# Kernel tuning notes

Hardware: AMD Instinct MI355X
Metric: run time of the kernel (lower is better)

Reference implementation:

```python
import jax, jax.numpy as jnp
import numpy as np

D_MODEL = 512; NHEAD = 8; D_FF = 2048
B = 8; C = 64; P = 128
HALF = D_MODEL // 2        # per-branch embed dim (256)
H_HALF = NHEAD // 2        # per-branch heads (4)
HD = HALF // H_HALF        # per-branch head dim (64)
ROPE_BASE = 10000.0
THETA_SCALE = 2.0 * np.pi
LN_EPS = 1e-5; RMS_EPS = 1e-8


def setup_inputs():
    ks = jax.random.split(jax.random.key(0), 16)
    w = lambda k, s: jax.random.normal(k, s, jnp.float32) * 0.02
    return {
        "src": jax.random.normal(ks[0], (B, C, P, D_MODEL), jnp.float32),
        "coords": jax.random.normal(ks[1], (C, 3), jnp.float32),
        "q_attn": w(ks[2], (D_MODEL,)), "rms_attn": jnp.ones((D_MODEL,), jnp.float32),
        "proj_attn_w": w(ks[3], (D_MODEL, D_MODEL)), "proj_attn_b": jnp.zeros((D_MODEL,), jnp.float32),
        "q_ffn": w(ks[4], (D_MODEL,)), "rms_ffn": jnp.ones((D_MODEL,), jnp.float32),
        "proj_ffn_w": w(ks[5], (D_MODEL, D_MODEL)), "proj_ffn_b": jnp.zeros((D_MODEL,), jnp.float32),
        "ln1_w": jnp.ones((D_MODEL,), jnp.float32), "ln1_b": jnp.zeros((D_MODEL,), jnp.float32),
        "ln2_w": jnp.ones((D_MODEL,), jnp.float32), "ln2_b": jnp.zeros((D_MODEL,), jnp.float32),
        "qkv_s_w": w(ks[6], (3 * HALF, HALF)), "qkv_s_b": jnp.zeros((3 * HALF,), jnp.float32),
        "out_s_w": w(ks[7], (HALF, HALF)), "out_s_b": jnp.zeros((HALF,), jnp.float32),
        "qkv_t_w": w(ks[8], (3 * HALF, HALF)), "qkv_t_b": jnp.zeros((3 * HALF,), jnp.float32),
        "out_t_w": w(ks[9], (HALF, HALF)), "out_t_b": jnp.zeros((HALF,), jnp.float32),
        "w1": w(ks[10], (D_FF, D_MODEL)), "b1": jnp.zeros((D_FF,), jnp.float32),
        "w2": w(ks[11], (D_MODEL, D_FF)), "b2": jnp.zeros((D_MODEL,), jnp.float32),
    }


def _rmsnorm(x, w):
    return x / jnp.sqrt(jnp.mean(x * x, axis=-1, keepdims=True) + RMS_EPS) * w


def _layernorm(x, w, b):
    m = jnp.mean(x, axis=-1, keepdims=True)
    v = jnp.mean((x - m) ** 2, axis=-1, keepdims=True)
    return (x - m) / jnp.sqrt(v + LN_EPS) * w + b


def _attn_residual(src, q, norm_w, proj_w, proj_b):
    # sources = [src] stacked on a leading n-axis (n=1) as in AttentionResidual
    V = src[None]                                  # (n, B, C, P, D)
    K = _rmsnorm(V, norm_w)
    logits = jnp.einsum('d,nbcpd->nbcp', q, K)
    wgt = jax.nn.softmax(logits, axis=0)
    out = jnp.einsum('nbcp,nbcpd->bcpd', wgt, V)
    return out @ proj_w.T + proj_b


def _build_freqs(half, dtype):
    idx = jnp.arange(half, dtype=dtype)
    return 1.0 / ROPE_BASE ** (idx / max(half, 1))


def _coord_rope(coords, half):
    # coords: (L, 3); returns cos, sin of shape (1, 1, L, half)
    axis_ids = jnp.arange(half) % 3
    c = coords - jnp.mean(coords, axis=0, keepdims=True)
    r = jnp.linalg.norm(c, axis=-1)
    c = c / jnp.maximum(jnp.max(r), 1e-6)
    freqs = _build_freqs(half, coords.dtype)
    theta = THETA_SCALE * (c[:, axis_ids] * freqs[None, :])   # (L, half)
    return jnp.cos(theta)[None, None], jnp.sin(theta)[None, None]


def _index_rope(L, half, dtype):
    freqs = _build_freqs(half, dtype)
    pos = jnp.arange(L, dtype=dtype)[:, None]
    theta = pos * freqs[None, :]                               # (L, half)
    return jnp.cos(theta)[None, None], jnp.sin(theta)[None, None]


def _apply_rope(q, k, cos, sin):
    half = q.shape[-1] // 2
    q1, q2 = q[..., :half], q[..., half:]
    k1, k2 = k[..., :half], k[..., half:]
    qr = jnp.concatenate([q1 * cos - q2 * sin, q1 * sin + q2 * cos], axis=-1)
    kr = jnp.concatenate([k1 * cos - k2 * sin, k1 * sin + k2 * cos], axis=-1)
    return qr, kr


def _mha(x, w_qkv, b_qkv, w_o, b_o, H, cos, sin):
    Bx, L, E = x.shape
    Hd = E // H
    qkv = x @ w_qkv.T + b_qkv
    q, k, v = jnp.split(qkv, 3, axis=-1)
    q = q.reshape(Bx, L, H, Hd).transpose(0, 2, 1, 3)   # (B, H, L, Hd)
    k = k.reshape(Bx, L, H, Hd).transpose(0, 2, 1, 3)
    v = v.reshape(Bx, L, H, Hd).transpose(0, 2, 1, 3)
    q, k = _apply_rope(q, k, cos, sin)
    scores = jnp.einsum('bhld,bhmd->bhlm', q, k) * (Hd ** -0.5)
    attn = jax.nn.softmax(scores, axis=-1)
    out = jnp.einsum('bhlm,bhmd->bhld', attn, v)
    out = out.transpose(0, 2, 1, 3).reshape(Bx, L, E)
    return out @ w_o.T + b_o


def reference(src, coords, q_attn, rms_attn, proj_attn_w, proj_attn_b,
              q_ffn, rms_ffn, proj_ffn_w, proj_ffn_b,
              ln1_w, ln1_b, ln2_w, ln2_b,
              qkv_s_w, qkv_s_b, out_s_w, out_s_b,
              qkv_t_w, qkv_t_b, out_t_w, out_t_b,
              w1, b1, w2, b2):
    Bx, Cx, Px, D = src.shape
    half = D // 2
    # --- attention block (pre-norm, attention-residual shortcut) ---
    res1 = _attn_residual(src, q_attn, rms_attn, proj_attn_w, proj_attn_b)
    x = _layernorm(src, ln1_w, ln1_b)
    # spatial branch: attention over channels with coordinate RoPE
    xs = x[..., :half].transpose(0, 2, 1, 3).reshape(Bx * Px, Cx, half)
    cos_s, sin_s = _coord_rope(coords, HD // 2)
    ys = _mha(xs, qkv_s_w, qkv_s_b, out_s_w, out_s_b, H_HALF, cos_s, sin_s)
    ys = ys.reshape(Bx, Px, Cx, half).transpose(0, 2, 1, 3)
    # temporal branch: attention over patches with index RoPE
    xt = x[..., half:].reshape(Bx * Cx, Px, half)
    cos_t, sin_t = _index_rope(Px, HD // 2, src.dtype)
    yt = _mha(xt, qkv_t_w, qkv_t_b, out_t_w, out_t_b, H_HALF, cos_t, sin_t)
    yt = yt.reshape(Bx, Cx, Px, half)
    x = res1 + jnp.concatenate([ys, yt], axis=-1)
    # --- FFN block ---
    res2 = _attn_residual(x, q_ffn, rms_ffn, proj_ffn_w, proj_ffn_b)
    y = _layernorm(x, ln2_w, ln2_b)
    ff = jax.nn.gelu(y @ w1.T + b1, approximate=False) @ w2.T + b2
    return res2 + ff
```

## Files before the change

### kernel.cpp

```cpp
#include <hip/hip_runtime.h>
#include <math.h>
#include <type_traits>

using u16 = unsigned short;
using u32 = unsigned int;

typedef __bf16 bf16x8 __attribute__((ext_vector_type(8)));
typedef float f32x4 __attribute__((ext_vector_type(4)));

__device__ __forceinline__ float lof(u32 u) { u32 x = u << 16; float f; __builtin_memcpy(&f, &x, 4); return f; }
__device__ __forceinline__ float hif(u32 u) { u32 x = u & 0xffff0000u; float f; __builtin_memcpy(&f, &x, 4); return f; }
__device__ __forceinline__ u16 f2bf(float f) {
  u32 u; __builtin_memcpy(&u, &f, 4);
  u32 r = u + 0x7fffu + ((u >> 16) & 1u);
  return (u16)(r >> 16);
}
__device__ __forceinline__ u32 pack2(float a, float b) { return (u32)f2bf(a) | ((u32)f2bf(b) << 16); }
__device__ __forceinline__ float bf2f(u16 s) { u32 x = ((u32)s) << 16; float f; __builtin_memcpy(&f, &x, 4); return f; }
__device__ __forceinline__ float elem(const u32* arr, int j) { u32 u = arr[j >> 1]; return (j & 1) ? hif(u) : lof(u); }

__device__ __forceinline__ void gload_lds16(const u16* g, u16* l) {
  __builtin_amdgcn_global_load_lds((const __attribute__((address_space(1))) void*)g,
                                   (__attribute__((address_space(3))) void*)l, 16, 0, 0);
}

__device__ __forceinline__ float gelu_f(float x) {
  float x3 = x * x * x;
  float u = fmaf(x3, 0.07135481283f, 1.5957691216f * x);
  float e = __expf(u);
  float r = __builtin_amdgcn_rcpf(e + 1.0f);
  return x * e * r;
}

#define NTOK 65536

#define WB_PA   0
#define WB_PF   262144
#define WB_QS   524288
#define WB_QT   720896
#define WB_OS   917504
#define WB_OT   983040
#define WB_W1   1048576
#define WB_W2F  2097152
#define WB_TOT  3407872

#define UC_US 0
#define UC_CS 768
#define UC_UT 1536
#define UC_CT 2304
#define UC_U1 3072
#define UC_C1 5120
#define UC_BC 7168

constexpr size_t O_WB  = 0;
constexpr size_t O_TAB = 6815744;
constexpr size_t O_ST1 = 6864896;
constexpr size_t O_ST2 = 7389184;
constexpr size_t O_UC  = 7913472;
constexpr size_t O_X   = 7944192;
constexpr size_t O_HB  = O_X + (size_t)NTOK * 512 * 2;

__global__ __launch_bounds__(256) void convert_weights_kernel(
    const float* __restrict__ pa, const float* __restrict__ pf,
    const float* __restrict__ qs, const float* __restrict__ qt,
    const float* __restrict__ os_, const float* __restrict__ ot,
    const float* __restrict__ w1, const float* __restrict__ w2,
    const float* __restrict__ ln1w, const float* __restrict__ ln2w,
    u16* __restrict__ dst)
{
  int i = blockIdx.x * 256 + threadIdx.x;
  if (i >= WB_TOT) return;
  float v;
  if (i < 262144)       { v = pa[i]; }
  else if (i < 524288)  { v = pf[i - 262144]; }
  else if (i < 720896)  { int l = i - 524288;  v = qs[l] * ln1w[l & 255]; }
  else if (i < 917504)  { int l = i - 720896;  v = qt[l] * ln1w[256 + (l & 255)]; }
  else if (i < 983040)  { v = os_[i - 917504]; }
  else if (i < 1048576) { v = ot[i - 983040]; }
  else if (i < 2097152) { int l = i - 1048576; v = w1[l] * ln2w[l & 511]; }
  else {
    int l = i - 2097152; int row = l / 2560, col = l - row * 2560;
    v = (col < 2048) ? w2[row * 2048 + col] : pf[row * 512 + (col - 2048)];
  }
  dst[i] = f2bf(v);
}

__global__ __launch_bounds__(256) void ucvec_kernel(
    const float* __restrict__ qs, const float* __restrict__ qt, const float* __restrict__ w1,
    const float* __restrict__ ln1w, const float* __restrict__ ln1b,
    const float* __restrict__ ln2w, const float* __restrict__ ln2b,
    const float* __restrict__ b2, const float* __restrict__ pfb,
    float* __restrict__ uc)
{
  int j = blockIdx.x * 256 + threadIdx.x;
  if (j < 768) {
    float u = 0.f, c = 0.f;
    for (int k = 0; k < 256; k++) { float w = qs[j * 256 + k]; u += ln1w[k] * w; c += ln1b[k] * w; }
    uc[UC_US + j] = u; uc[UC_CS + j] = c;
  } else if (j < 1536) {
    int jj = j - 768; float u = 0.f, c = 0.f;
    for (int k = 0; k < 256; k++) { float w = qt[jj * 256 + k]; u += ln1w[256 + k] * w; c += ln1b[256 + k] * w; }
    uc[UC_UT + jj] = u; uc[UC_CT + jj] = c;
  } else if (j < 3584) {
    int jj = j - 1536; float u = 0.f, c = 0.f;
    for (int k = 0; k < 512; k++) { float w = w1[jj * 512 + k]; u += ln2w[k] * w; c += ln2b[k] * w; }
    uc[UC_U1 + jj] = u; uc[UC_C1 + jj] = c;
  } else if (j < 4096) {
    int jj = j - 3584;
    uc[UC_BC + jj] = b2[jj] + pfb[jj];
  }
}

__global__ __launch_bounds__(256) void rope_tables_kernel(const float* __restrict__ coords, float* __restrict__ tab)
{
  __shared__ float cs[192];
  __shared__ float mean3[3];
  __shared__ float rmax;
  int t = threadIdx.x;
  if (t < 192) cs[t] = coords[t];
  __syncthreads();
  if (t < 3) { float s = 0.f; for (int i = 0; i < 64; i++) s += cs[i * 3 + t]; mean3[t] = s * (1.0f / 64.0f); }
  __syncthreads();
  if (t < 192) cs[t] -= mean3[t % 3];
  __syncthreads();
  if (t == 0) {
    float mx = 0.f;
    for (int i = 0; i < 64; i++) {
      float x = cs[i * 3], y = cs[i * 3 + 1], z = cs[i * 3 + 2];
      mx = fmaxf(mx, sqrtf(x * x + y * y + z * z));
    }
    rmax = fmaxf(mx, 1e-6f);
  }
  __syncthreads();
  float inv = 1.0f / rmax;
  for (int e = t; e < 2048; e += 256) {
    int c = e >> 5, j = e & 31;
    float freq = 1.0f / powf(10000.0f, (float)j * (1.0f / 32.0f));
    float th = 6.283185307179586f * (cs[c * 3 + (j % 3)] * inv) * freq;
    tab[e] = cosf(th); tab[2048 + e] = sinf(th);
  }
  for (int e = t; e < 4096; e += 256) {
    int p = e >> 5, j = e & 31;
    float freq = 1.0f / powf(10000.0f, (float)j * (1.0f / 32.0f));
    float th = (float)p * freq;
    tab[4096 + e] = cosf(th); tab[8192 + e] = sinf(th);
  }
}

__global__ __launch_bounds__(256) void ln_stats_f32_kernel(
    const float* __restrict__ xin, float2* __restrict__ st, u16* __restrict__ srcb)
{
  const int tok = blockIdx.x * 4 + (threadIdx.x >> 6);
  const int lane = threadIdx.x & 63;
  const float* row = xin + (size_t)tok * 512 + lane * 8;
  float4 v0 = ((const float4*)row)[0];
  float4 v1 = ((const float4*)row)[1];
  float v[8] = {v0.x, v0.y, v0.z, v0.w, v1.x, v1.y, v1.z, v1.w};
  float s = 0.f, ss = 0.f;
#pragma unroll
  for (int j = 0; j < 8; j++) { s += v[j]; ss += v[j] * v[j]; }
#pragma unroll
  for (int o = 32; o > 0; o >>= 1) { s += __shfl_xor(s, o); ss += __shfl_xor(ss, o); }
  if (lane == 0) {
    float mean = s * (1.0f / 512.0f);
    float rstd = rsqrtf(ss * (1.0f / 512.0f) - mean * mean + 1e-5f);
    st[tok] = make_float2(mean, rstd);
  }
  if (srcb) {
    uint4 o; u32* op = (u32*)&o;
#pragma unroll
    for (int d = 0; d < 4; d++) op[d] = pack2(v[2 * d], v[2 * d + 1]);
    *(uint4*)(srcb + (size_t)tok * 512 + lane * 8) = o;
  }
}

__global__ __launch_bounds__(256) void ln_stats_bf16_kernel(const u16* __restrict__ xin, float2* __restrict__ st)
{
  const int tok = blockIdx.x * 4 + (threadIdx.x >> 6);
  const int lane = threadIdx.x & 63;
  uint4 u = ((const uint4*)(xin + (size_t)tok * 512))[lane];
  u32 uu[4] = {u.x, u.y, u.z, u.w};
  float s = 0.f, ss = 0.f;
#pragma unroll
  for (int d = 0; d < 4; d++) {
    float a = lof(uu[d]), b = hif(uu[d]);
    s += a + b; ss += a * a + b * b;
  }
#pragma unroll
  for (int o = 32; o > 0; o >>= 1) { s += __shfl_xor(s, o); ss += __shfl_xor(ss, o); }
  if (lane == 0) {
    float mean = s * (1.0f / 512.0f);
    float rstd = rsqrtf(ss * (1.0f / 512.0f) - mean * mean + 1e-5f);
    st[tok] = make_float2(mean, rstd);
  }
}

template<int EMODE, typename OutT>
__global__ __launch_bounds__(256) void gemm128_kernel(
    const u16* __restrict__ A16, int lda,
    const u16* __restrict__ Wt, int ldw,
    OutT* __restrict__ C, int ldc,
    const float* __restrict__ bias,
    const float2* __restrict__ stats,
    const float* __restrict__ uvec, const float* __restrict__ cvec,
    int K)
{
  const int t = threadIdx.x;
  const int lane = t & 63, wid = t >> 6;
  const int wm = wid >> 1, wn = wid & 1;
  const int l15 = lane & 15, l4 = lane >> 4;

  const int ntn = gridDim.x;
  const int nwg = ntn * gridDim.y;
  int flat = blockIdx.y * ntn + blockIdx.x;
  int q = nwg >> 3, rmd = nwg & 7, xcd = flat & 7, idx = flat >> 3;
  int wg = (xcd < rmd ? xcd * (q + 1) : rmd * (q + 1) + (xcd - rmd) * q) + idx;
  const int m0 = (wg / ntn) * 128, n0 = (wg % ntn) * 128;

  f32x4 acc[4][4] = {};
  const int r0 = t >> 2;
  const size_t arow0 = (size_t)(m0 + r0);

  __shared__ u16 Asb[2][128 * 32];
  __shared__ u16 Bsb[2][128 * 32];
  const int chs = (t & 3) ^ ((t >> 3) & 3);
  const u16* Wp = Wt + (size_t)(n0 + r0) * ldw + chs * 8;
  const size_t wstep = (size_t)64 * ldw;
  const int nt = K / 32;
  auto stage = [&](int ti, int buf) {
    const int kk = ti * 32;
    const u16* pa = A16 + arow0 * lda + kk + chs * 8;
    const size_t rstep = (size_t)64 * lda;
    gload_lds16(pa, &Asb[buf][t * 8]);
    gload_lds16(pa + rstep, &Asb[buf][t * 8 + 2048]);
    gload_lds16(Wp + kk, &Bsb[buf][t * 8]);
    gload_lds16(Wp + wstep + kk, &Bsb[buf][t * 8 + 2048]);
  };
  stage(0, 0);
  int cur = 0;
  const int pco = (l4 ^ ((l15 >> 1) & 3)) * 8;
  for (int ti = 0; ti < nt; ti++) {
    if (ti + 1 < nt) {
      stage(ti + 1, cur ^ 1);
      __builtin_amdgcn_sched_barrier(0);
      asm volatile("s_waitcnt vmcnt(4)" ::: "memory");
    } else {
      __builtin_amdgcn_sched_barrier(0);
      asm volatile("s_waitcnt vmcnt(0)" ::: "memory");
    }
    __builtin_amdgcn_sched_barrier(0);
    __builtin_amdgcn_s_barrier();
    __builtin_amdgcn_sched_barrier(0);
    bf16x8 af[4], bfr[4];
#pragma unroll
    for (int i = 0; i < 4; i++)
      af[i] = *(const bf16x8*)(&Asb[cur][(wm * 64 + i * 16 + l15) * 32 + pco]);
#pragma unroll
    for (int j = 0; j < 4; j++)
      bfr[j] = *(const bf16x8*)(&Bsb[cur][(wn * 64 + j * 16 + l15) * 32 + pco]);
#pragma unroll
    for (int i = 0; i < 4; i++)
#pragma unroll
      for (int j = 0; j < 4; j++)
        acc[i][j] = __builtin_amdgcn_mfma_f32_16x16x32_bf16(af[i], bfr[j], acc[i][j], 0, 0, 0);
    __builtin_amdgcn_sched_barrier(0);
    __builtin_amdgcn_s_barrier();
    __builtin_amdgcn_sched_barrier(0);
    cur ^= 1;
  }

#pragma unroll
  for (int i = 0; i < 4; i++) {
    const int row = m0 + wm * 64 + i * 16 + l4 * 4;
#pragma unroll
    for (int j = 0; j < 4; j++) {
      const int col = n0 + wn * 64 + j * 16 + l15;
      const float bv = bias[col];
#pragma unroll
      for (int rr = 0; rr < 4; rr++) {
        float v = acc[i][j][rr];
        if constexpr (EMODE == 3) {
          float2 s = stats[row + rr];
          v = s.y * v - s.x * s.y * uvec[col] + cvec[col] + bv;
        } else {
          v += bv;
        }
        const size_t idxc = (size_t)(row + rr) * ldc + col;
        if constexpr (std::is_same<OutT, u16>::value) {
          if constexpr (EMODE == 2) v += bf2f(C[idxc]);
          C[idxc] = f2bf(v);
        } else {
          if constexpr (EMODE == 2) v += C[idxc];
          C[idxc] = v;
        }
      }
    }
  }
}

template<int AMODE, int EMODE, typename OutT>
__global__ __launch_bounds__(512, 2) void gemm256_kernel(
    const u16* __restrict__ A16, int lda,
    const u16* __restrict__ A2, int lda2,
    const u16* __restrict__ Wt, int ldw,
    OutT* __restrict__ C, int ldc,
    const float* __restrict__ bias,
    const float2* __restrict__ stats,
    const float* __restrict__ uvec, const float* __restrict__ cvec,
    int K)
{
  __shared__ u16 As[3][256 * 32];
  __shared__ u16 Bs[3][256 * 32];
  const int t = threadIdx.x;
  const int lane = t & 63, wid = t >> 6;
  const int wm = wid >> 2, wn = wid & 3;
  const int l15 = lane & 15, l4 = lane >> 4;
  const int r0 = t >> 2;
  const int chs = (t & 3) ^ ((t >> 3) & 3);

  const int ntn = gridDim.x;
  const int nwg = ntn * gridDim.y;
  int flat = blockIdx.y * ntn + blockIdx.x;
  int q = nwg >> 3, rmd = nwg & 7, xcd = flat & 7, idx = flat >> 3;
  int wg = (xcd < rmd ? xcd * (q + 1) : rmd * (q + 1) + (xcd - rmd) * q) + idx;
  const int m0 = (wg / ntn) * 256, n0 = (wg % ntn) * 256;

  f32x4 acc[8][4] = {};

  const size_t arow0 = (size_t)(m0 + r0);
  const u16* Wp = Wt + (size_t)(n0 + r0) * ldw + chs * 8;
  const size_t wstep = (size_t)128 * ldw;
  const int nt = K >> 5;

  auto stage = [&](int ti, int buf) {
    const int kk = ti << 5;
    const int cbk = kk + chs * 8;
    const u16* pa; size_t rstep;
    if constexpr (AMODE == 4) {
      if (kk < 2048) { pa = A16 + arow0 * lda + cbk;          rstep = (size_t)128 * lda; }
      else           { pa = A2 + arow0 * lda2 + (cbk - 2048); rstep = (size_t)128 * lda2; }
    } else {
      pa = A16 + arow0 * lda + cbk; rstep = (size_t)128 * lda;
    }
    gload_lds16(pa,         &As[buf][t * 8]);
    gload_lds16(pa + rstep, &As[buf][t * 8 + 4096]);
    gload_lds16(Wp + kk,          &Bs[buf][t * 8]);
    gload_lds16(Wp + wstep + kk,  &Bs[buf][t * 8 + 4096]);
  };

  stage(0, 0);
  stage(1, 1);
  const int pco = (l4 ^ ((l15 >> 1) & 3)) * 8;
  int cb = 0;
  for (int ti = 0; ti < nt; ti++) {
    __builtin_amdgcn_sched_barrier(0);
    if (ti + 1 < nt) { asm volatile("s_waitcnt vmcnt(4)" ::: "memory"); }
    else             { asm volatile("s_waitcnt vmcnt(0)" ::: "memory"); }
    __builtin_amdgcn_sched_barrier(0);
    __builtin_amdgcn_s_barrier();
    __builtin_amdgcn_sched_barrier(0);
    if (ti + 2 < nt) {
      int b2 = cb + 2; if (b2 >= 3) b2 -= 3;
      stage(ti + 2, b2);
    }
    bf16x8 af[8], bfr[4];
#pragma unroll
    for (int i = 0; i < 8; i++)
      af[i] = *(const bf16x8*)(&As[cb][(wm * 128 + i * 16 + l15) * 32 + pco]);
#pragma unroll
    for (int j = 0; j < 4; j++)
      bfr[j] = *(const bf16x8*)(&Bs[cb][(wn * 64 + j * 16 + l15) * 32 + pco]);
    __builtin_amdgcn_s_setprio(1);
#pragma unroll
    for (int i = 0; i < 8; i++)
#pragma unroll
      for (int j = 0; j < 4; j++)
        acc[i][j] = __builtin_amdgcn_mfma_f32_16x16x32_bf16(af[i], bfr[j], acc[i][j], 0, 0, 0);
    __builtin_amdgcn_s_setprio(0);
    __builtin_amdgcn_sched_barrier(0);
    cb = cb == 2 ? 0 : cb + 1;
  }

  auto epi = [&](float v, int row, int col) -> float {
    const float bv = bias[col];
    if constexpr (EMODE >= 3) {
      float2 s = stats[row];
      v = s.y * v - s.x * s.y * uvec[col] + cvec[col] + bv;
      if constexpr (EMODE == 4) v = gelu_f(v);
    } else {
      v += bv;
    }
    return v;
  };

  if constexpr (std::is_same<OutT, u16>::value) {
    __syncthreads();
    u16* sl = &As[0][0] + wid * 3072;
    const int lr = lane >> 3;
    const int lcb = (lane & 7) * 8;
#pragma unroll
    for (int cc = 0; cc < 4; cc++) {
#pragma unroll
      for (int ii = 0; ii < 2; ii++) {
        const int i = cc * 2 + ii;
        const int rbase = m0 + wm * 128 + i * 16 + l4 * 4;
#pragma unroll
        for (int j = 0; j < 4; j++) {
          const int col = n0 + wn * 64 + j * 16 + l15;
#pragma unroll
          for (int rr = 0; rr < 4; rr++) {
            float v = epi(acc[i][j][rr], rbase + rr, col);
            sl[(ii * 16 + l4 * 4 + rr) * 66 + j * 16 + l15] = f2bf(v);
          }
        }
      }
#pragma unroll
      for (int ps = 0; ps < 4; ps++) {
        const int r = ps * 8 + lr;
        uint4 d = *(const uint4*)(sl + r * 66 + lcb);
        const int grow = m0 + wm * 128 + cc * 32 + r;
        *(uint4*)(C + (size_t)grow * ldc + n0 + wn * 64 + lcb) = d;
      }
    }
  } else {
#pragma unroll
    for (int i = 0; i < 8; i++) {
      const int row = m0 + wm * 128 + i * 16 + l4 * 4;
#pragma unroll
      for (int j = 0; j < 4; j++) {
        const int col = n0 + wn * 64 + j * 16 + l15;
#pragma unroll
        for (int rr = 0; rr < 4; rr++) {
          float v = epi(acc[i][j][rr], row + rr, col);
          C[(size_t)(row + rr) * ldc + col] = v;
        }
      }
    }
  }
}

template<int EMODE, typename OutT>
__global__ __launch_bounds__(256) void gemm_f32a_kernel(
    const float* __restrict__ A32, int lda,
    const u16* __restrict__ Wt, int ldw,
    OutT* __restrict__ C, int ldc,
    const float* __restrict__ bias,
    const float2* __restrict__ stats,
    const float* __restrict__ uvec, const float* __restrict__ cvec,
    int K)
{
  const int t = threadIdx.x;
  const int lane = t & 63, wid = t >> 6;
  const int wm = wid >> 1, wn = wid & 1;
  const int l15 = lane & 15, l4 = lane >> 4;
  const int r0 = t >> 2;
  const int ntn = gridDim.x;
  const int nwg = ntn * gridDim.y;
  int flat = blockIdx.y * ntn + blockIdx.x;
  int q = nwg >> 3, rmd = nwg & 7, xcd = flat & 7, idx = flat >> 3;
  int wg = (xcd < rmd ? xcd * (q + 1) : rmd * (q + 1) + (xcd - rmd) * q) + idx;
  const int m0 = (wg / ntn) * 128, n0 = (wg % ntn) * 128;
  f32x4 acc[4][4] = {};
  const size_t arow0 = (size_t)(m0 + r0);
  const int ch = t & 3;
  const u16* Wp = Wt + (size_t)(n0 + r0) * ldw + ch * 8;
  const size_t wstep = (size_t)64 * ldw;
  __shared__ u16 As[128 * 40];
  __shared__ u16 Bs[128 * 32];
  for (int k0 = 0; k0 < K; k0 += 32) {
    const int cbx = k0 + ch * 8;
    uint4 a0, a1;
    float f0[8], f1[8];
    float4 x0 = *(const float4*)(A32 + arow0 * lda + cbx);
    float4 x1 = *(const float4*)(A32 + arow0 * lda + cbx + 4);
    float4 y0 = *(const float4*)(A32 + (arow0 + 64) * lda + cbx);
    float4 y1 = *(const float4*)(A32 + (arow0 + 64) * lda + cbx + 4);
    f0[0]=x0.x; f0[1]=x0.y; f0[2]=x0.z; f0[3]=x0.w; f0[4]=x1.x; f0[5]=x1.y; f0[6]=x1.z; f0[7]=x1.w;
    f1[0]=y0.x; f1[1]=y0.y; f1[2]=y0.z; f1[3]=y0.w; f1[4]=y1.x; f1[5]=y1.y; f1[6]=y1.z; f1[7]=y1.w;
    u32* p0 = (u32*)&a0; u32* p1 = (u32*)&a1;
#pragma unroll
    for (int d = 0; d < 4; d++) { p0[d] = pack2(f0[2*d], f0[2*d+1]); p1[d] = pack2(f1[2*d], f1[2*d+1]); }
    __syncthreads();
    gload_lds16(Wp + k0, Bs + t * 8);
    gload_lds16(Wp + wstep + k0, Bs + t * 8 + 2048);
    *(uint4*)(As + r0 * 40 + ch * 8) = a0;
    *(uint4*)(As + (r0 + 64) * 40 + ch * 8) = a1;
    __syncthreads();
    bf16x8 af[4], bfr[4];
#pragma unroll
    for (int i = 0; i < 4; i++)
      af[i] = *(const bf16x8*)(As + (wm * 64 + i * 16 + l15) * 40 + l4 * 8);
#pragma unroll
    for (int j = 0; j < 4; j++)
      bfr[j] = *(const bf16x8*)(Bs + (wn * 64 + j * 16 + l15) * 32 + l4 * 8);
#pragma unroll
    for (int i = 0; i < 4; i++)
#pragma unroll
      for (int j = 0; j < 4; j++)
        acc[i][j] = __builtin_amdgcn_mfma_f32_16x16x32_bf16(af[i], bfr[j], acc[i][j], 0, 0, 0);
  }
#pragma unroll
  for (int i = 0; i < 4; i++) {
    const int row = m0 + wm * 64 + i * 16 + l4 * 4;
#pragma unroll
    for (int j = 0; j < 4; j++) {
      const int col = n0 + wn * 64 + j * 16 + l15;
      const float bv = bias[col];
#pragma unroll
      for (int rr = 0; rr < 4; rr++) {
        float v = acc[i][j][rr];
        if constexpr (EMODE == 3) {
          float2 s = stats[row + rr];
          v = s.y * v - s.x * s.y * uvec[col] + cvec[col] + bv;
        } else {
          v += bv;
        }
        const size_t idxc = (size_t)(row + rr) * ldc + col;
        if constexpr (std::is_same<OutT, u16>::value) C[idxc] = f2bf(v);
        else C[idxc] = v;
      }
    }
  }
}

template<int L>
__global__ __launch_bounds__(256) void attn_mfma_kernel(
    const u16* __restrict__ qkv,
    u16* __restrict__ aout,
    const float* __restrict__ tab)
{
  constexpr int KP = 72;
  constexpr int PP = L + 8;
  constexpr int VP = L + 8;
  constexpr int NI = L / 64;
  constexpr int NJ = L / 16;
  constexpr int NK = L / 32;
  __shared__ u16 Ks[L * KP];
  __shared__ u16 Vt[64 * VP];
  __shared__ u16 Ps[L * PP];

  const int t = threadIdx.x;
  const int lane = t & 63;
  const int w = t >> 6;
  const int l15 = lane & 15, l4 = lane >> 4;
  const int sq = blockIdx.x, h = blockIdx.y;

  long base; int tstride; const float *ct, *st;
  if constexpr (L == 64) { base = (long)(sq >> 7) * 8192 + (sq & 127); tstride = 128; ct = tab;        st = tab + 2048; }
  else                   { base = (long)sq * 128;                      tstride = 1;   ct = tab + 4096; st = tab + 8192; }

  {
    const int tok = t >> 1, hh = t & 1;
    if (tok < L) {
      const size_t rb = (size_t)(base + (long)tok * tstride) * 768 + h * 64;
      u32 ku[32];
#pragma unroll
      for (int i = 0; i < 8; i++) ((uint4*)ku)[i] = ((const uint4*)(qkv + rb + 256))[i];
      const float* cc = ct + tok * 32;
      const float* ss = st + tok * 32;
      u32* kd = (u32*)(Ks + tok * KP + hh * 32);
#pragma unroll
      for (int jj = 0; jj < 16; jj++) {
        float c0 = cc[2*jj], s0 = ss[2*jj], c1 = cc[2*jj+1], s1 = ss[2*jj+1];
        float a0 = elem(ku, 2*jj),     b0 = elem(ku, 2*jj+32);
        float a1 = elem(ku, 2*jj+1),   b1 = elem(ku, 2*jj+33);
        float r0v = hh ? (a0*s0 + b0*c0) : (a0*c0 - b0*s0);
        float r1v = hh ? (a1*s1 + b1*c1) : (a1*c1 - b1*s1);
        kd[jj] = pack2(r0v, r1v);
      }
      u32 vu[16];
#pragma unroll
      for (int i = 0; i < 4; i++) ((uint4*)vu)[i] = ((const uint4*)(qkv + rb + 512 + hh * 32))[i];
#pragma unroll
      for (int j = 0; j < 32; j++)
        Vt[(hh * 32 + j) * VP + tok] = (u16)(vu[j >> 1] >> ((j & 1) * 16));
    }
  }

  bf16x8 aq[NI][2];
#pragma unroll
  for (int i = 0; i < NI; i++) {
    const int row = w * (16 * NI) + i * 16 + l15;
    const u16* qr = qkv + (size_t)(base + (long)row * tstride) * 768 + h * 64;
    uint4 ua = *(const uint4*)(qr + l4 * 8);
    uint4 ub = *(const uint4*)(qr + 32 + l4 * 8);
    u32 au[4] = {ua.x, ua.y, ua.z, ua.w};
    u32 bu[4] = {ub.x, ub.y, ub.z, ub.w};
    const float* cc = ct + row * 32 + l4 * 8;
    const float* ss = st + row * 32 + l4 * 8;
    u32 q0[4], q1[4];
#pragma unroll
    for (int d = 0; d < 4; d++) {
      float a0 = lof(au[d]), a1 = hif(au[d]);
      float b0 = lof(bu[d]), b1 = hif(bu[d]);
      float c0 = cc[2*d], c1 = cc[2*d+1], s0 = ss[2*d], s1 = ss[2*d+1];
      q0[d] = pack2(a0*c0 - b0*s0, a1*c1 - b1*s1);
      q1[d] = pack2(a0*s0 + b0*c0, a1*s1 + b1*c1);
    }
    __builtin_memcpy(&aq[i][0], q0, 16);
    __builtin_memcpy(&aq[i][1], q1, 16);
  }
  __syncthreads();

  f32x4 acc[NI][NJ] = {};
#pragma unroll
  for (int j = 0; j < NJ; j++) {
#pragma unroll
    for (int kk = 0; kk < 2; kk++) {
      bf16x8 bk = *(const bf16x8*)(Ks + (j * 16 + l15) * KP + kk * 32 + l4 * 8);
#pragma unroll
      for (int i = 0; i < NI; i++)
        acc[i][j] = __builtin_amdgcn_mfma_f32_16x16x32_bf16(aq[i][kk], bk, acc[i][j], 0, 0, 0);
    }
  }

  float inv_[NI][4];
#pragma unroll
  for (int i = 0; i < NI; i++) {
#pragma unroll
    for (int rr = 0; rr < 4; rr++) {
      float m = acc[i][0][rr];
#pragma unroll
      for (int j = 1; j < NJ; j++) m = fmaxf(m, acc[i][j][rr]);
      m = fmaxf(m, __shfl_xor(m, 1)); m = fmaxf(m, __shfl_xor(m, 2));
      m = fmaxf(m, __shfl_xor(m, 4)); m = fmaxf(m, __shfl_xor(m, 8));
      m *= 0.125f;
      const int qrow = w * (16 * NI) + i * 16 + l4 * 4 + rr;
      float sm = 0.f;
#pragma unroll
      for (int j = 0; j < NJ; j++) {
        float e = __expf(acc[i][j][rr] * 0.125f - m);
        sm += e;
        Ps[qrow * PP + j * 16 + l15] = f2bf(e);
      }
      sm += __shfl_xor(sm, 1); sm += __shfl_xor(sm, 2);
      sm += __shfl_xor(sm, 4); sm += __shfl_xor(sm, 8);
      inv_[i][rr] = 1.0f / sm;
    }
  }

  f32x4 o[NI][4] = {};
#pragma unroll
  for (int kk = 0; kk < NK; kk++) {
    bf16x8 pa[NI];
#pragma unroll
    for (int i = 0; i < NI; i++)
      pa[i] = *(const bf16x8*)(Ps + (w * (16 * NI) + i * 16 + l15) * PP + kk * 32 + l4 * 8);
#pragma unroll
    for (int jn = 0; jn < 4; jn++) {
      bf16x8 bv = *(const bf16x8*)(Vt + (jn * 16 + l15) * VP + kk * 32 + l4 * 8);
#pragma unroll
      for (int i = 0; i < NI; i++)
        o[i][jn] = __builtin_amdgcn_mfma_f32_16x16x32_bf16(pa[i], bv, o[i][jn], 0, 0, 0);
    }
  }

#pragma unroll
  for (int i = 0; i < NI; i++) {
#pragma unroll
    for (int rr = 0; rr < 4; rr++) {
      const int qrow = w * (16 * NI) + i * 16 + l4 * 4 + rr;
      u16* op = aout + (size_t)(base + (long)qrow * tstride) * 256 + h * 64;
      const float iv = inv_[i][rr];
#pragma unroll
      for (int jn = 0; jn < 4; jn++)
        op[jn * 16 + l15] = f2bf(o[i][jn][rr] * iv);
    }
  }
}

extern "C" void kernel_launch(void* const* d_in, const int* in_sizes, int n_in,
                              void* d_out, int out_size, void* d_ws, size_t ws_size,
                              hipStream_t stream) {
  const float* src         = (const float*)d_in[0];
  const float* coords      = (const float*)d_in[1];
  const float* proj_attn_w = (const float*)d_in[4];
  const float* proj_attn_b = (const float*)d_in[5];
  const float* proj_ffn_w  = (const float*)d_in[8];
  const float* proj_ffn_b  = (const float*)d_in[9];
  const float* ln1_w = (const float*)d_in[10];
  const float* ln1_b = (const float*)d_in[11];
  const float* ln2_w = (const float*)d_in[12];
  const float* ln2_b = (const float*)d_in[13];
  const float* qkv_s_w = (const float*)d_in[14];
  const float* qkv_s_b = (const float*)d_in[15];
  const float* out_s_w = (const float*)d_in[16];
  const float* out_s_b = (const float*)d_in[17];
  const float* qkv_t_w = (const float*)d_in[18];
  const float* qkv_t_b = (const float*)d_in[19];
  const float* out_t_w = (const float*)d_in[20];
  const float* out_t_b = (const float*)d_in[21];
  const float* w1 = (const float*)d_in[22];
  const float* b1 = (const float*)d_in[23];
  const float* w2 = (const float*)d_in[24];
  const float* b2 = (const float*)d_in[25];
  float* out = (float*)d_out;
  char* ws = (char*)d_ws;

  const size_t srcb_bytes = (size_t)NTOK * 512 * 2;
  const int tiers[7] = {65536, 32768, 16384, 8192, 4096, 2048, 512};
  int crows = 0; bool fast = false;
  for (int i = 0; i < 7; i++) {
    size_t need = O_HB + (size_t)tiers[i] * 2048 * 2 + srcb_bytes;
    if (ws_size >= need) { crows = tiers[i]; fast = true; break; }
  }
  if (!crows) {
    for (int i = 0; i < 7; i++)
      if (ws_size >= O_HB + (size_t)tiers[i] * 2048 * 2) { crows = tiers[i]; break; }
  }
  if (!crows) return;
  size_t o_srcb = O_HB + (size_t)crows * 2048 * 2;

  u16*    wb  = (u16*)(ws + O_WB);
  float*  tab = (float*)(ws + O_TAB);
  float2* st1 = (float2*)(ws + O_ST1);
  float2* st2 = (float2*)(ws + O_ST2);
  float*  uc  = (float*)(ws + O_UC);
  u16*    x   = (u16*)(ws + O_X);
  u16*    hb  = (u16*)(ws + O_HB);
  u16*    srcb = fast ? (u16*)(ws + o_srcb) : nullptr;

  u16* qkvb  = (u16*)d_out;
  u16* aoutb = (u16*)((char*)d_out + (size_t)NTOK * 768 * 2);

  convert_weights_kernel<<<(WB_TOT + 255) / 256, 256, 0, stream>>>(
      proj_attn_w, proj_ffn_w, qkv_s_w, qkv_t_w, out_s_w, out_t_w, w1, w2, ln1_w, ln2_w, wb);
  ucvec_kernel<<<16, 256, 0, stream>>>(qkv_s_w, qkv_t_w, w1, ln1_w, ln1_b, ln2_w, ln2_b, b2, proj_ffn_b, uc);
  rope_tables_kernel<<<1, 256, 0, stream>>>(coords, tab);
  ln_stats_f32_kernel<<<NTOK / 4, 256, 0, stream>>>(src, st1, srcb);

  if (fast)
    gemm128_kernel<0, u16><<<dim3(4, 512), 256, 0, stream>>>(srcb, 512, wb + WB_PA, 512, x, 512, proj_attn_b, nullptr, nullptr, nullptr, 512);
  else
    gemm_f32a_kernel<0, u16><<<dim3(4, 512), 256, 0, stream>>>(src, 512, wb + WB_PA, 512, x, 512, proj_attn_b, nullptr, nullptr, nullptr, 512);

  if (fast)
    gemm128_kernel<3, u16><<<dim3(6, 512), 256, 0, stream>>>(srcb, 512, wb + WB_QS, 256, qkvb, 768, qkv_s_b, st1, uc + UC_US, uc + UC_CS, 256);
  else
    gemm_f32a_kernel<3, u16><<<dim3(6, 512), 256, 0, stream>>>(src, 512, wb + WB_QS, 256, qkvb, 768, qkv_s_b, st1, uc + UC_US, uc + UC_CS, 256);
  attn_mfma_kernel<64><<<dim3(1024, 4), 256, 0, stream>>>(qkvb, aoutb, tab);
  gemm128_kernel<2, u16><<<dim3(2, 512), 256, 0, stream>>>(aoutb, 256, wb + WB_OS, 256, x, 512, out_s_b, nullptr, nullptr, nullptr, 256);

  if (fast)
    gemm128_kernel<3, u16><<<dim3(6, 512), 256, 0, stream>>>(srcb + 256, 512, wb + WB_QT, 256, qkvb, 768, qkv_t_b, st1, uc + UC_UT, uc + UC_CT, 256);
  else
    gemm_f32a_kernel<3, u16><<<dim3(6, 512), 256, 0, stream>>>(src + 256, 512, wb + WB_QT, 256, qkvb, 768, qkv_t_b, st1, uc + UC_UT, uc + UC_CT, 256);
  attn_mfma_kernel<128><<<dim3(512, 4), 256, 0, stream>>>(qkvb, aoutb, tab);
  gemm128_kernel<2, u16><<<dim3(2, 512), 256, 0, stream>>>(aoutb, 256, wb + WB_OT, 256, x + 256, 512, out_t_b, nullptr, nullptr, nullptr, 256);

  ln_stats_bf16_kernel<<<NTOK / 4, 256, 0, stream>>>(x, st2);

  for (int r = 0; r < NTOK; r += crows) {
    gemm256_kernel<0, 4, u16><<<dim3(8, crows / 256), 512, 0, stream>>>(
        x + (size_t)r * 512, 512, nullptr, 0, wb + WB_W1, 512, hb, 2048, b1, st2 + r, uc + UC_U1, uc + UC_C1, 512);
    gemm256_kernel<4, 0, float><<<dim3(2, crows / 256), 512, 0, stream>>>(
        hb, 2048, x + (size_t)r * 512, 512, wb + WB_W2F, 2560, out + (size_t)r * 512, 512, uc + UC_BC, nullptr, nullptr, nullptr, 2560);
  }
}
```

Measured before the change: 968.7 us.

## Restructure 256x256 FFN GEMM into K=64 double-buffered, 8-phase interleaved pipeline

The FFN GEMM kernel now stages 64-wide K tiles in two LDS buffers instead of 32-wide tiles in three. Each iteration is split into four barrier-separated MFMA phases, and the next tile's A and B loads are issued between phases to overlap global-to-LDS traffic with compute. The XOR swizzle is widened to 8 chunks to match the 64-element rows. The bf16 epilogue's LDS-staged vectorized store path is removed in favor of direct scalar stores. The extra barriers, the full vmcnt(0) wait each iteration, and the scalar bf16 stores of the large hidden activation may offset the gains.

```diff
diff --git a/kernel.cpp b/kernel.cpp
--- a/kernel.cpp
+++ b/kernel.cpp
@@ -299,7 +299,7 @@
 }
 
 template<int AMODE, int EMODE, typename OutT>
-__global__ __launch_bounds__(512, 2) void gemm256_kernel(
+__global__ __launch_bounds__(512, 2) void gemm8p_kernel(
     const u16* __restrict__ A16, int lda,
     const u16* __restrict__ A2, int lda2,
     const u16* __restrict__ Wt, int ldw,
@@ -309,14 +309,12 @@
     const float* __restrict__ uvec, const float* __restrict__ cvec,
     int K)
 {
-  __shared__ u16 As[3][256 * 32];
-  __shared__ u16 Bs[3][256 * 32];
+  __shared__ u16 As[2][256 * 64];
+  __shared__ u16 Bs[2][256 * 64];
   const int t = threadIdx.x;
   const int lane = t & 63, wid = t >> 6;
   const int wm = wid >> 2, wn = wid & 3;
   const int l15 = lane & 15, l4 = lane >> 4;
-  const int r0 = t >> 2;
-  const int chs = (t & 3) ^ ((t >> 3) & 3);
 
   const int ntn = gridDim.x;
   const int nwg = ntn * gridDim.y;
@@ -327,113 +325,136 @@
 
   f32x4 acc[8][4] = {};
 
-  const size_t arow0 = (size_t)(m0 + r0);
-  const u16* Wp = Wt + (size_t)(n0 + r0) * ldw + chs * 8;
-  const size_t wstep = (size_t)128 * ldw;
-  const int nt = K >> 5;
-
-  auto stage = [&](int ti, int buf) {
-    const int kk = ti << 5;
-    const int cbk = kk + chs * 8;
-    const u16* pa; size_t rstep;
+  const int srow = t >> 3;
+  const int sch8 = ((t & 7) ^ (srow & 7)) * 8;
+  const u16* Wbase = Wt + (size_t)(n0 + srow) * ldw + sch8;
+
+  auto stageA = [&](int ti2, int buf) {
+    const int kk2 = ti2 << 6;
+    const u16* pa; size_t ld; int kb = kk2;
     if constexpr (AMODE == 4) {
-      if (kk < 2048) { pa = A16 + arow0 * lda + cbk;          rstep = (size_t)128 * lda; }
-      else           { pa = A2 + arow0 * lda2 + (cbk - 2048); rstep = (size_t)128 * lda2; }
-    } else {
-      pa = A16 + arow0 * lda + cbk; rstep = (size_t)128 * lda;
-    }
-    gload_lds16(pa,         &As[buf][t * 8]);
-    gload_lds16(pa + rstep, &As[buf][t * 8 + 4096]);
-    gload_lds16(Wp + kk,          &Bs[buf][t * 8]);
-    gload_lds16(Wp + wstep + kk,  &Bs[buf][t * 8 + 4096]);
+      if (kk2 < 2048) { pa = A16; ld = (size_t)lda; }
+      else            { pa = A2;  ld = (size_t)lda2; kb = kk2 - 2048; }
+    } else { pa = A16; ld = (size_t)lda; }
+    const u16* p = pa + (size_t)(m0 + srow) * ld + kb + sch8;
+    u16* d = &As[buf][t * 8];
+#pragma unroll
+    for (int l = 0; l < 4; l++)
+      gload_lds16(p + (size_t)(l * 64) * ld, d + l * 4096);
   };
-
-  stage(0, 0);
-  stage(1, 1);
-  const int pco = (l4 ^ ((l15 >> 1) & 3)) * 8;
-  int cb = 0;
+  auto stageB = [&](int ti2, int buf) {
+    const u16* p = Wbase + (ti2 << 6);
+    u16* d = &Bs[buf][t * 8];
+#pragma unroll
+    for (int l = 0; l < 4; l++)
+      gload_lds16(p + (size_t)(l * 64) * ldw, d + l * 4096);
+  };
+
+  const int nt = K >> 6;
+  stageA(0, 0); stageB(0, 0);
+
+  const int s7 = l15 & 7;
+  const int xc0 = (l4 ^ s7) * 8;
+  const int xc1 = ((4 + l4) ^ s7) * 8;
+  const int aoff = (wm * 128 + l15) * 64;
+  const int boff = (wn * 64 + l15) * 64;
+
+  int cbuf = 0;
   for (int ti = 0; ti < nt; ti++) {
     __builtin_amdgcn_sched_barrier(0);
-    if (ti + 1 < nt) { asm volatile("s_waitcnt vmcnt(4)" ::: "memory"); }
-    else             { asm volatile("s_waitcnt vmcnt(0)" ::: "memory"); }
+    asm volatile("s_waitcnt vmcnt(0)" ::: "memory");
     __builtin_amdgcn_sched_barrier(0);
     __builtin_amdgcn_s_barrier();
     __builtin_amdgcn_sched_barrier(0);
-    if (ti + 2 < nt) {
-      int b2 = cb + 2; if (b2 >= 3) b2 -= 3;
-      stage(ti + 2, b2);
-    }
-    bf16x8 af[8], bfr[4];
-#pragma unroll
-    for (int i = 0; i < 8; i++)
-      af[i] = *(const bf16x8*)(&As[cb][(wm * 128 + i * 16 + l15) * 32 + pco]);
+    const u16* Ab = &As[cbuf][0];
+    const u16* Bb = &Bs[cbuf][0];
+    bf16x8 af[4], bfr[4];
+
+    if (ti + 1 < nt) stageA(ti + 1, cbuf ^ 1);
+#pragma unroll
+    for (int ii = 0; ii < 4; ii++)
+      af[ii] = *(const bf16x8*)(Ab + aoff + ii * 1024 + xc0);
 #pragma unroll
     for (int j = 0; j < 4; j++)
-      bfr[j] = *(const bf16x8*)(&Bs[cb][(wn * 64 + j * 16 + l15) * 32 + pco]);
+      bfr[j] = *(const bf16x8*)(Bb + boff + j * 1024 + xc0);
     __builtin_amdgcn_s_setprio(1);
 #pragma unroll
-    for (int i = 0; i < 8; i++)
+    for (int ii = 0; ii < 4; ii++)
 #pragma unroll
       for (int j = 0; j < 4; j++)
-        acc[i][j] = __builtin_amdgcn_mfma_f32_16x16x32_bf16(af[i], bfr[j], acc[i][j], 0, 0, 0);
+        acc[ii][j] = __builtin_amdgcn_mfma_f32_16x16x32_bf16(af[ii], bfr[j], acc[ii][j], 0, 0, 0);
     __builtin_amdgcn_s_setprio(0);
     __builtin_amdgcn_sched_barrier(0);
-    cb = cb == 2 ? 0 : cb + 1;
-  }
-
-  auto epi = [&](float v, int row, int col) -> float {
-    const float bv = bias[col];
-    if constexpr (EMODE >= 3) {
-      float2 s = stats[row];
-      v = s.y * v - s.x * s.y * uvec[col] + cvec[col] + bv;
-      if constexpr (EMODE == 4) v = gelu_f(v);
-    } else {
-      v += bv;
-    }
-    return v;
-  };
-
-  if constexpr (std::is_same<OutT, u16>::value) {
-    __syncthreads();
-    u16* sl = &As[0][0] + wid * 3072;
-    const int lr = lane >> 3;
-    const int lcb = (lane & 7) * 8;
-#pragma unroll
-    for (int cc = 0; cc < 4; cc++) {
-#pragma unroll
-      for (int ii = 0; ii < 2; ii++) {
-        const int i = cc * 2 + ii;
-        const int rbase = m0 + wm * 128 + i * 16 + l4 * 4;
-#pragma unroll
-        for (int j = 0; j < 4; j++) {
-          const int col = n0 + wn * 64 + j * 16 + l15;
-#pragma unroll
-          for (int rr = 0; rr < 4; rr++) {
-            float v = epi(acc[i][j][rr], rbase + rr, col);
-            sl[(ii * 16 + l4 * 4 + rr) * 66 + j * 16 + l15] = f2bf(v);
-          }
+    __builtin_amdgcn_s_barrier();
+    __builtin_amdgcn_sched_barrier(0);
+
+    if (ti + 1 < nt) stageB(ti + 1, cbuf ^ 1);
+#pragma unroll
+    for (int ii = 0; ii < 4; ii++)
+      af[ii] = *(const bf16x8*)(Ab + aoff + 4096 + ii * 1024 + xc0);
+    __builtin_amdgcn_s_setprio(1);
+#pragma unroll
+    for (int ii = 0; ii < 4; ii++)
+#pragma unroll
+      for (int j = 0; j < 4; j++)
+        acc[4 + ii][j] = __builtin_amdgcn_mfma_f32_16x16x32_bf16(af[ii], bfr[j], acc[4 + ii][j], 0, 0, 0);
+    __builtin_amdgcn_s_setprio(0);
+    __builtin_amdgcn_sched_barrier(0);
+    __builtin_amdgcn_s_barrier();
+    __builtin_amdgcn_sched_barrier(0);
+
+#pragma unroll
+    for (int ii = 0; ii < 4; ii++)
+      af[ii] = *(const bf16x8*)(Ab + aoff + ii * 1024 + xc1);
+#pragma unroll
+    for (int j = 0; j < 4; j++)
+      bfr[j] = *(const bf16x8*)(Bb + boff + j * 1024 + xc1);
+    __builtin_amdgcn_s_setprio(1);
+#pragma unroll
+    for (int ii = 0; ii < 4; ii++)
+#pragma unroll
+      for (int j = 0; j < 4; j++)
+        acc[ii][j] = __builtin_amdgcn_mfma_f32_16x16x32_bf16(af[ii], bfr[j], acc[ii][j], 0, 0, 0);
+    __builtin_amdgcn_s_setprio(0);
+    __builtin_amdgcn_sched_barrier(0);
+    __builtin_amdgcn_s_barrier();
+    __builtin_amdgcn_sched_barrier(0);
+
+#pragma unroll
+    for (int ii = 0; ii < 4; ii++)
+      af[ii] = *(const bf16x8*)(Ab + aoff + 4096 + ii * 1024 + xc1);
+    __builtin_amdgcn_s_setprio(1);
+#pragma unroll
+    for (int ii = 0; ii < 4; ii++)
+#pragma unroll
+      for (int j = 0; j < 4; j++)
+        acc[4 + ii][j] = __builtin_amdgcn_mfma_f32_16x16x32_bf16(af[ii], bfr[j], acc[4 + ii][j], 0, 0, 0);
+    __builtin_amdgcn_s_setprio(0);
+    __builtin_amdgcn_sched_barrier(0);
+
+    cbuf ^= 1;
+  }
+
+#pragma unroll
+  for (int i = 0; i < 8; i++) {
+    const int row = m0 + wm * 128 + i * 16 + l4 * 4;
+#pragma unroll
+    for (int j = 0; j < 4; j++) {
+      const int col = n0 + wn * 64 + j * 16 + l15;
+      const float bv = bias[col];
+#pragma unroll
+      for (int rr = 0; rr < 4; rr++) {
+        float v = acc[i][j][rr];
+        if constexpr (EMODE == 4) {
+          float2 s = stats[row + rr];
+          v = s.y * v - s.x * s.y * uvec[col] + cvec[col] + bv;
+          v = gelu_f(v);
+        } else {
+          v += bv;
         }
-      }
-#pragma unroll
-      for (int ps = 0; ps < 4; ps++) {
-        const int r = ps * 8 + lr;
-        uint4 d = *(const uint4*)(sl + r * 66 + lcb);
-        const int grow = m0 + wm * 128 + cc * 32 + r;
-        *(uint4*)(C + (size_t)grow * ldc + n0 + wn * 64 + lcb) = d;
-      }
-    }
-  } else {
-#pragma unroll
-    for (int i = 0; i < 8; i++) {
-      const int row = m0 + wm * 128 + i * 16 + l4 * 4;
-#pragma unroll
-      for (int j = 0; j < 4; j++) {
-        const int col = n0 + wn * 64 + j * 16 + l15;
-#pragma unroll
-        for (int rr = 0; rr < 4; rr++) {
-          float v = epi(acc[i][j][rr], row + rr, col);
-          C[(size_t)(row + rr) * ldc + col] = v;
-        }
+        const size_t idxc = (size_t)(row + rr) * ldc + col;
+        if constexpr (std::is_same<OutT, u16>::value) C[idxc] = f2bf(v);
+        else C[idxc] = v;
       }
     }
   }
@@ -751,9 +772,9 @@
   ln_stats_bf16_kernel<<<NTOK / 4, 256, 0, stream>>>(x, st2);
 
   for (int r = 0; r < NTOK; r += crows) {
-    gemm256_kernel<0, 4, u16><<<dim3(8, crows / 256), 512, 0, stream>>>(
+    gemm8p_kernel<0, 4, u16><<<dim3(8, crows / 256), 512, 0, stream>>>(
         x + (size_t)r * 512, 512, nullptr, 0, wb + WB_W1, 512, hb, 2048, b1, st2 + r, uc + UC_U1, uc + UC_C1, 512);
-    gemm256_kernel<4, 0, float><<<dim3(2, crows / 256), 512, 0, stream>>>(
+    gemm8p_kernel<4, 0, float><<<dim3(2, crows / 256), 512, 0, stream>>>(
         hb, 2048, x + (size_t)r * 512, 512, wb + WB_W2F, 2560, out + (size_t)r * 512, 512, uc + UC_BC, nullptr, nullptr, nullptr, 2560);
   }
 }
```

New measurement: 964.5 us. About the same (-0.4%).
